# Kernel optimization log

Hardware: AMD Instinct MI355X
Metric: run time of the kernel (lower is better)

Reference implementation:

```python
import jax, jax.numpy as jnp
import numpy as np

NUM_VARS = 64
LAG = 16
H1 = 64
H2 = 1024
NUM_OUT = 1
BATCH = 16384


def setup_inputs() -> dict:
    key = jax.random.key(0)
    ks = jax.random.split(key, 8)

    def xavier(k, shape, fan_in, fan_out):
        std = float(np.sqrt(2.0 / (fan_in + fan_out)))
        return jax.random.normal(k, shape, dtype=jnp.float32) * std

    inputs = jax.random.normal(ks[0], (BATCH, NUM_VARS * LAG), dtype=jnp.float32)
    # Per-variable sub-network weights, batched over the variable axis.
    W1 = xavier(ks[1], (NUM_VARS, LAG, H1), LAG, H1)
    b1 = jnp.full((NUM_VARS, H1), 0.1, dtype=jnp.float32)
    W2 = xavier(ks[2], (NUM_VARS, H1, H1), H1, H1)
    b2 = jnp.full((NUM_VARS, H1), 0.1, dtype=jnp.float32)
    imp = (jnp.ones((NUM_VARS,), dtype=jnp.float32) / NUM_VARS
           + 1e-5 * jax.random.normal(ks[3], (NUM_VARS,), dtype=jnp.float32))
    W3 = xavier(ks[4], (NUM_VARS * H1, H2), NUM_VARS * H1, H2)
    b3 = jnp.full((H2,), 0.1, dtype=jnp.float32)
    W4 = xavier(ks[5], (H2, NUM_OUT), H2, NUM_OUT)
    b4 = jnp.full((NUM_OUT,), 0.1, dtype=jnp.float32)
    return {"inputs": inputs, "W1": W1, "b1": b1, "W2": W2, "b2": b2,
            "imp": imp, "W3": W3, "b3": b3, "W4": W4, "b4": b4}


def reference(inputs, W1, b1, W2, b2, imp, W3, b3, W4, b4):
    B = inputs.shape[0]
    # [B, V*lag] -> [B, V, lag]; slicing inputs[:, lag*i:lag*(i+1)] == x[:, i, :]
    x = inputs.reshape(B, NUM_VARS, LAG)
    # dp = 0.0 -> dropout is identity
    h = jax.nn.relu(jnp.einsum('bvl,vlh->bvh', x, W1) + b1[None])      # [B, V, H1]
    h = jax.nn.relu(jnp.einsum('bvh,vhk->bvk', h, W2) + b2[None])      # [B, V, H1]
    agg = (h * imp[None, :, None]).reshape(B, NUM_VARS * H1)            # weighted concat
    pred = jax.nn.relu(agg @ W3 + b3) @ W4 + b4                        # [B, NUM_OUT]
    return pred
```

## Files before the change

### kernel.cpp

```cpp
#include <hip/hip_runtime.h>
#include <hip/hip_bf16.h>
#include <stdint.h>

#define B_ROWS 16384
#define NVARS 64
#define LAG 16
#define H1 64
#define H2 1024
#define KDIM (NVARS * H1)

typedef __attribute__((ext_vector_type(8))) short short8;
typedef __attribute__((ext_vector_type(4))) short short4v;
typedef __attribute__((ext_vector_type(4))) float f32x4;

typedef __attribute__((address_space(3))) uint8_t lds_u8;
typedef const __attribute__((address_space(1))) uint8_t glob_u8;

__device__ __forceinline__ void gload_lds16(const void* g, void* l) {
    __builtin_amdgcn_global_load_lds((glob_u8*)g, (lds_u8*)l, 16, 0, 0);
}

__device__ __forceinline__ short f2bf_s(float x) {
    __hip_bfloat16 h = __float2bfloat16(x);
    return *(short*)&h;
}
__device__ __forceinline__ float bf_s2f(short s) {
    __hip_bfloat16 h = *(__hip_bfloat16*)&s;
    return __bfloat162float(h);
}

__global__ __launch_bounds__(256) void misc_pre_kernel(
    const float* __restrict__ w3, const float* __restrict__ b4,
    const float* __restrict__ W1, const float* __restrict__ W2,
    __hip_bfloat16* __restrict__ w3t, float* __restrict__ out,
    short* __restrict__ w1bh, short* __restrict__ w1bl,
    short* __restrict__ w2bh, short* __restrict__ w2bl) {
    __shared__ float tile[64][65];
    const int bid = blockIdx.x;
    const int t = threadIdx.x;

    if (bid < 1024) {
        const int k0 = (bid >> 4) * 64;
        const int n0 = (bid & 15) * 64;
        const int c = t & 63, r0 = t >> 6;
#pragma unroll
        for (int i = 0; i < 16; i++) {
            int r = r0 + i * 4;
            tile[r][c] = w3[(size_t)(k0 + r) * H2 + n0 + c];
        }
        __syncthreads();
#pragma unroll
        for (int i = 0; i < 16; i++) {
            int nr = r0 + i * 4;
            w3t[(size_t)(n0 + nr) * KDIM + k0 + c] = __float2bfloat16(tile[c][nr]);
        }
        return;
    }
    if (bid < 1088) {
        out[(bid - 1024) * 256 + t] = b4[0];
        return;
    }

    const int v = bid - 1088;
    for (int idx = t; idx < 64 * 32; idx += 256) {
        int col = idx >> 5, k = idx & 31;
        float wv = W1[((size_t)v * LAG + (k & 15)) * H1 + col];
        short hi = f2bf_s(wv);
        w1bh[((size_t)v * 64 + col) * 40 + k] = hi;
        w1bl[((size_t)v * 64 + col) * 40 + k] = (k < 16) ? f2bf_s(wv - bf_s2f(hi)) : (short)0;
    }
    for (int idx = t; idx < 64 * 64; idx += 256) {
        int col = idx >> 6, k = idx & 63;
        float wv = W2[((size_t)v * H1 + k) * H1 + col];
        short hi = f2bf_s(wv);
        w2bh[((size_t)v * 64 + col) * 72 + k] = hi;
        w2bl[((size_t)v * 64 + col) * 72 + k] = f2bf_s(wv - bf_s2f(hi));
    }
}

__global__ __launch_bounds__(256) void subnets_mfma_kernel(
    const float* __restrict__ inputs, const float* __restrict__ b1g,
    const float* __restrict__ b2g, const float* __restrict__ impg,
    const short* __restrict__ w1bh_g, const short* __restrict__ w1bl_g,
    const short* __restrict__ w2bh_g, const short* __restrict__ w2bl_g,
    __hip_bfloat16* __restrict__ agg) {
    const int v = blockIdx.x >> 7;
    const int b0 = (blockIdx.x & 127) * 128;
    const int t = threadIdx.x;
    const int lane = t & 63, wv = t >> 6;
    const int l15 = lane & 15, g = lane >> 4;

    __shared__ __align__(16) char smem[38912];
    short* xsS   = (short*)smem;
    short* w1bhS = (short*)(smem + 10240);
    short* w1blS = (short*)(smem + 15360);
    short* Hs    = (short*)smem;
    short* w2bhS = (short*)(smem + 20480);
    short* w2blS = (short*)(smem + 29696);

    for (int c = t; c < 320; c += 256) {
        gload_lds16(w1bh_g + (size_t)v * 2560 + c * 8, (char*)w1bhS + c * 16);
        gload_lds16(w1bl_g + (size_t)v * 2560 + c * 8, (char*)w1blS + c * 16);
    }
    for (int c = t; c < 576; c += 256) {
        gload_lds16(w2bh_g + (size_t)v * 4608 + c * 8, (char*)w2bhS + c * 16);
        gload_lds16(w2bl_g + (size_t)v * 4608 + c * 8, (char*)w2blS + c * 16);
    }
#pragma unroll
    for (int i = 0; i < 2; i++) {
        int idx = t + i * 256;
        int row = idx >> 2, seg = idx & 3;
        float4 x4 = *(const float4*)(inputs + (size_t)(b0 + row) * (NVARS * LAG) + v * LAG + seg * 4);
        const float* xp = (const float*)&x4;
        short4v hv, lv;
#pragma unroll
        for (int j = 0; j < 4; j++) {
            short hi = f2bf_s(xp[j]);
            hv[j] = hi;
            lv[j] = f2bf_s(xp[j] - bf_s2f(hi));
        }
        *(short4v*)&xsS[row * 40 + seg * 4] = hv;
        *(short4v*)&xsS[row * 40 + 16 + seg * 4] = lv;
    }
    __syncthreads();

    short8 a1[2], b1hF[4], b1lF[4];
#pragma unroll
    for (int mt = 0; mt < 2; mt++)
        a1[mt] = *(const short8*)&xsS[(wv * 32 + mt * 16 + l15) * 40 + g * 8];
#pragma unroll
    for (int nt = 0; nt < 4; nt++) {
        b1hF[nt] = *(const short8*)&w1bhS[(nt * 16 + l15) * 40 + g * 8];
        b1lF[nt] = *(const short8*)&w1blS[(nt * 16 + l15) * 40 + g * 8];
    }
    f32x4 acc1[2][4];
#pragma unroll
    for (int mt = 0; mt < 2; mt++)
#pragma unroll
        for (int nt = 0; nt < 4; nt++) {
            acc1[mt][nt] = (f32x4){0.f, 0.f, 0.f, 0.f};
            acc1[mt][nt] = __builtin_amdgcn_mfma_f32_16x16x32_bf16(a1[mt], b1hF[nt], acc1[mt][nt], 0, 0, 0);
            acc1[mt][nt] = __builtin_amdgcn_mfma_f32_16x16x32_bf16(a1[mt], b1lF[nt], acc1[mt][nt], 0, 0, 0);
        }
    __syncthreads();

#pragma unroll
    for (int mt = 0; mt < 2; mt++)
#pragma unroll
        for (int nt = 0; nt < 4; nt++) {
            int col = nt * 16 + l15;
            float bias = b1g[v * H1 + col];
#pragma unroll
            for (int r = 0; r < 4; r++) {
                float h = fmaxf(acc1[mt][nt][r] + bias, 0.f);
                int row = wv * 32 + mt * 16 + g * 4 + r;
                Hs[row * 72 + col] = f2bf_s(h);
            }
        }
    __syncthreads();

    short8 a2[2][2], b2hF[4][2], b2lF[4][2];
#pragma unroll
    for (int mt = 0; mt < 2; mt++)
#pragma unroll
        for (int kc = 0; kc < 2; kc++)
            a2[mt][kc] = *(const short8*)&Hs[(wv * 32 + mt * 16 + l15) * 72 + kc * 32 + g * 8];
#pragma unroll
    for (int nt = 0; nt < 4; nt++)
#pragma unroll
        for (int kc = 0; kc < 2; kc++) {
            b2hF[nt][kc] = *(const short8*)&w2bhS[(nt * 16 + l15) * 72 + kc * 32 + g * 8];
            b2lF[nt][kc] = *(const short8*)&w2blS[(nt * 16 + l15) * 72 + kc * 32 + g * 8];
        }
    f32x4 acc2[2][4];
#pragma unroll
    for (int mt = 0; mt < 2; mt++)
#pragma unroll
        for (int nt = 0; nt < 4; nt++) {
            f32x4 a = (f32x4){0.f, 0.f, 0.f, 0.f};
            a = __builtin_amdgcn_mfma_f32_16x16x32_bf16(a2[mt][0], b2hF[nt][0], a, 0, 0, 0);
            a = __builtin_amdgcn_mfma_f32_16x16x32_bf16(a2[mt][1], b2hF[nt][1], a, 0, 0, 0);
            a = __builtin_amdgcn_mfma_f32_16x16x32_bf16(a2[mt][0], b2lF[nt][0], a, 0, 0, 0);
            a = __builtin_amdgcn_mfma_f32_16x16x32_bf16(a2[mt][1], b2lF[nt][1], a, 0, 0, 0);
            acc2[mt][nt] = a;
        }

    const float impv = impg[v];
#pragma unroll
    for (int mt = 0; mt < 2; mt++)
#pragma unroll
        for (int nt = 0; nt < 4; nt++) {
            int col = nt * 16 + l15;
            float bias = b2g[v * H1 + col];
#pragma unroll
            for (int r = 0; r < 4; r++) {
                float o = fmaxf(acc2[mt][nt][r] + bias, 0.f) * impv;
                int row = b0 + wv * 32 + mt * 16 + g * 4 + r;
                agg[(size_t)row * KDIM + v * H1 + col] = __float2bfloat16(o);
            }
        }
}

#define NT 128

__global__ __launch_bounds__(512, 2) void gemm3_kernel(
    const __hip_bfloat16* __restrict__ agg,
    const __hip_bfloat16* __restrict__ w3t,
    const float* __restrict__ b3, const float* __restrict__ W4,
    float* __restrict__ out) {
    const int bid = ((blockIdx.x & 7) << 5) + (blockIdx.x >> 3);
    const int brow = (bid >> 2) * 256;
    const int bcol = (bid & 3) * 256;
    const int t = threadIdx.x;
    const int lane = t & 63;
    const int wid = t >> 6;
    const int wm = wid >> 2, wn = wid & 3;
    const int l15 = lane & 15, g = lane >> 4;

    __shared__ __align__(16) char smem[131072];

    const int c0 = t, c1 = t + 512;
    const int r0 = c0 >> 2, r1 = c1 >> 2;
    const int col0 = ((c0 & 3) * 8) ^ ((r0 & 8) ? 16 : 0);
    const int col1 = ((c1 & 3) * 8) ^ ((r1 & 8) ? 16 : 0);
    const __hip_bfloat16* aS0 = agg + (size_t)(brow + r0) * KDIM + col0;
    const __hip_bfloat16* aS1 = agg + (size_t)(brow + r1) * KDIM + col1;
    const __hip_bfloat16* bS0 = w3t + (size_t)(bcol + r0) * KDIM + col0;
    const __hip_bfloat16* bS1 = w3t + (size_t)(bcol + r1) * KDIM + col1;

#define STAGE_AB(p, kt) do { \
        gload_lds16(aS0 + (kt) * 32, smem + (p) * 32768 + c0 * 16); \
        gload_lds16(aS1 + (kt) * 32, smem + (p) * 32768 + c1 * 16); \
        gload_lds16(bS0 + (kt) * 32, smem + (p) * 32768 + 16384 + c0 * 16); \
        gload_lds16(bS1 + (kt) * 32, smem + (p) * 32768 + 16384 + c1 * 16); } while (0)

    const int coff = (g * 16) ^ ((l15 & 8) ? 32 : 0);
    const int aBase = (wm * 128 + l15) * 64 + coff;
    const int bBase = 16384 + (wn * 64 + l15) * 64 + coff;

#define RD(p, off) (*(const short8*)(smem + (p) * 32768 + (off)))
#define LDFRAGS(FA, FB, p) do { \
        FA[0] = RD(p, aBase + 0 * 1024); FA[1] = RD(p, aBase + 1 * 1024); \
        FA[2] = RD(p, aBase + 2 * 1024); FA[3] = RD(p, aBase + 3 * 1024); \
        FA[4] = RD(p, aBase + 4 * 1024); FA[5] = RD(p, aBase + 5 * 1024); \
        FA[6] = RD(p, aBase + 6 * 1024); FA[7] = RD(p, aBase + 7 * 1024); \
        FB[0] = RD(p, bBase + 0 * 1024); FB[1] = RD(p, bBase + 1 * 1024); \
        FB[2] = RD(p, bBase + 2 * 1024); FB[3] = RD(p, bBase + 3 * 1024); } while (0)

#define MM(FA, FB) do { \
        __builtin_amdgcn_s_setprio(1); \
        _Pragma("unroll") \
        for (int mm = 0; mm < 8; mm++) \
            _Pragma("unroll") \
            for (int nn = 0; nn < 4; nn++) \
                acc[mm][nn] = __builtin_amdgcn_mfma_f32_16x16x32_bf16( \
                    FA[mm], FB[nn], acc[mm][nn], 0, 0, 0); \
        __builtin_amdgcn_s_setprio(0); } while (0)

#define TILE(FAc, FBc, FAn, FBn, tn, DOPREF, DOSTAGE, kt3, VMSTR) do { \
        if (DOPREF) LDFRAGS(FAn, FBn, (tn) & 3); \
        if (DOSTAGE) STAGE_AB((kt3) & 3, kt3); \
        MM(FAc, FBc); \
        asm volatile(VMSTR ::: "memory"); \
        __builtin_amdgcn_s_barrier(); \
        __builtin_amdgcn_sched_barrier(0); } while (0)

    short8 fa0[8], fb0[4], fa1[8], fb1[4];
    f32x4 acc[8][4];
#pragma unroll
    for (int m = 0; m < 8; m++)
#pragma unroll
        for (int n = 0; n < 4; n++) acc[m][n] = (f32x4){0.f, 0.f, 0.f, 0.f};

    STAGE_AB(0, 0);
    STAGE_AB(1, 1);
    STAGE_AB(2, 2);
    asm volatile("s_waitcnt vmcnt(4)" ::: "memory");
    __builtin_amdgcn_s_barrier();
    __builtin_amdgcn_sched_barrier(0);
    LDFRAGS(fa0, fb0, 0);

#pragma unroll 4
    for (int tt = 0; tt < NT - 4; ++tt) {
        if (tt & 1) TILE(fa1, fb1, fa0, fb0, tt + 1, 1, 1, tt + 3, "s_waitcnt vmcnt(4)");
        else        TILE(fa0, fb0, fa1, fb1, tt + 1, 1, 1, tt + 3, "s_waitcnt vmcnt(4)");
    }
    TILE(fa0, fb0, fa1, fb1, 125, 1, 1, 127, "s_waitcnt vmcnt(4)");
    TILE(fa1, fb1, fa0, fb0, 126, 1, 0, 0,   "s_waitcnt vmcnt(0)");
    TILE(fa0, fb0, fa1, fb1, 127, 1, 0, 0,   "s_waitcnt vmcnt(0)");
    MM(fa1, fb1);

    float bias[4], w4v[4];
#pragma unroll
    for (int n = 0; n < 4; n++) {
        int col = bcol + wn * 64 + n * 16 + l15;
        bias[n] = b3[col];
        w4v[n] = W4[col];
    }
#pragma unroll
    for (int m = 0; m < 8; m++) {
        float pr0 = 0.f, pr1 = 0.f, pr2 = 0.f, pr3 = 0.f;
#pragma unroll
        for (int n = 0; n < 4; n++) {
            pr0 += fmaxf(acc[m][n][0] + bias[n], 0.f) * w4v[n];
            pr1 += fmaxf(acc[m][n][1] + bias[n], 0.f) * w4v[n];
            pr2 += fmaxf(acc[m][n][2] + bias[n], 0.f) * w4v[n];
            pr3 += fmaxf(acc[m][n][3] + bias[n], 0.f) * w4v[n];
        }
#pragma unroll
        for (int mask = 1; mask < 16; mask <<= 1) {
            pr0 += __shfl_xor(pr0, mask, 64);
            pr1 += __shfl_xor(pr1, mask, 64);
            pr2 += __shfl_xor(pr2, mask, 64);
            pr3 += __shfl_xor(pr3, mask, 64);
        }
        if (l15 == 0) {
            int row = brow + wm * 128 + m * 16 + g * 4;
            atomicAdd(&out[row + 0], pr0);
            atomicAdd(&out[row + 1], pr1);
            atomicAdd(&out[row + 2], pr2);
            atomicAdd(&out[row + 3], pr3);
        }
    }
}

extern "C" void kernel_launch(void* const* d_in, const int* in_sizes, int n_in,
                              void* d_out, int out_size, void* d_ws, size_t ws_size,
                              hipStream_t stream) {
    const float* inputs = (const float*)d_in[0];
    const float* W1 = (const float*)d_in[1];
    const float* b1 = (const float*)d_in[2];
    const float* W2 = (const float*)d_in[3];
    const float* b2 = (const float*)d_in[4];
    const float* imp = (const float*)d_in[5];
    const float* W3 = (const float*)d_in[6];
    const float* b3 = (const float*)d_in[7];
    const float* W4 = (const float*)d_in[8];
    const float* b4 = (const float*)d_in[9];
    float* out = (float*)d_out;

    char* ws = (char*)d_ws;
    const size_t agg_bytes = (size_t)B_ROWS * KDIM * 2;
    const size_t w3t_bytes = (size_t)H2 * KDIM * 2;
    const size_t w1b_bytes = (size_t)NVARS * 64 * 40 * 2;
    const size_t w2b_bytes = (size_t)NVARS * 64 * 72 * 2;

    __hip_bfloat16* agg = (__hip_bfloat16*)ws;
    __hip_bfloat16* w3t = (__hip_bfloat16*)(ws + agg_bytes);
    short* w1bh = (short*)(ws + agg_bytes + w3t_bytes);
    short* w1bl = (short*)(ws + agg_bytes + w3t_bytes + w1b_bytes);
    short* w2bh = (short*)(ws + agg_bytes + w3t_bytes + 2 * w1b_bytes);
    short* w2bl = (short*)(ws + agg_bytes + w3t_bytes + 2 * w1b_bytes + w2b_bytes);

    hipLaunchKernelGGL(misc_pre_kernel, dim3(1152), dim3(256), 0, stream,
                       W3, b4, W1, W2, w3t, out, w1bh, w1bl, w2bh, w2bl);
    hipLaunchKernelGGL(subnets_mfma_kernel, dim3(NVARS * (B_ROWS / 128)), dim3(256), 0, stream,
                       inputs, b1, b2, imp, w1bh, w1bl, w2bh, w2bl, agg);
    hipLaunchKernelGGL(gemm3_kernel, dim3((B_ROWS / 256) * (H2 / 256)), dim3(512), 0, stream,
                       agg, w3t, b3, W4, out);
}
```

Measured before the change: 183.8 us.

## Load GEMM3 B fragments directly from global into registers, halve LDS staging

The W3 operand is no longer staged through LDS. Each wave now loads its B fragments straight from global memory into registers, two k-tiles ahead, while only the A tile keeps the 4-stage LDS ring, which halves shared memory to 64KB. A-fragment register double-buffering is dropped: A fragments are read from LDS right before each MFMA batch. The aim is to cut LDS traffic and footprint. The cost is uncoalesced-ish global loads for B, duplicated across the wm waves, and LDS read latency exposed with no prefetch.

Result: slower. 223.8 us (+21.8%).

```diff
diff --git a/kernel.cpp b/kernel.cpp
--- a/kernel.cpp
+++ b/kernel.cpp
@@ -217,7 +217,7 @@
     const int wm = wid >> 2, wn = wid & 3;
     const int l15 = lane & 15, g = lane >> 4;
 
-    __shared__ __align__(16) char smem[131072];
+    __shared__ __align__(16) char smem[65536];
 
     const int c0 = t, c1 = t + 512;
     const int r0 = c0 >> 2, r1 = c1 >> 2;
@@ -225,70 +225,69 @@
     const int col1 = ((c1 & 3) * 8) ^ ((r1 & 8) ? 16 : 0);
     const __hip_bfloat16* aS0 = agg + (size_t)(brow + r0) * KDIM + col0;
     const __hip_bfloat16* aS1 = agg + (size_t)(brow + r1) * KDIM + col1;
-    const __hip_bfloat16* bS0 = w3t + (size_t)(bcol + r0) * KDIM + col0;
-    const __hip_bfloat16* bS1 = w3t + (size_t)(bcol + r1) * KDIM + col1;
-
-#define STAGE_AB(p, kt) do { \
-        gload_lds16(aS0 + (kt) * 32, smem + (p) * 32768 + c0 * 16); \
-        gload_lds16(aS1 + (kt) * 32, smem + (p) * 32768 + c1 * 16); \
-        gload_lds16(bS0 + (kt) * 32, smem + (p) * 32768 + 16384 + c0 * 16); \
-        gload_lds16(bS1 + (kt) * 32, smem + (p) * 32768 + 16384 + c1 * 16); } while (0)
+
+#define STAGE_A(p, kt) do { \
+        gload_lds16(aS0 + (kt) * 32, smem + (p) * 16384 + c0 * 16); \
+        gload_lds16(aS1 + (kt) * 32, smem + (p) * 16384 + c1 * 16); } while (0)
 
     const int coff = (g * 16) ^ ((l15 & 8) ? 32 : 0);
     const int aBase = (wm * 128 + l15) * 64 + coff;
-    const int bBase = 16384 + (wn * 64 + l15) * 64 + coff;
-
-#define RD(p, off) (*(const short8*)(smem + (p) * 32768 + (off)))
-#define LDFRAGS(FA, FB, p) do { \
-        FA[0] = RD(p, aBase + 0 * 1024); FA[1] = RD(p, aBase + 1 * 1024); \
-        FA[2] = RD(p, aBase + 2 * 1024); FA[3] = RD(p, aBase + 3 * 1024); \
-        FA[4] = RD(p, aBase + 4 * 1024); FA[5] = RD(p, aBase + 5 * 1024); \
-        FA[6] = RD(p, aBase + 6 * 1024); FA[7] = RD(p, aBase + 7 * 1024); \
-        FB[0] = RD(p, bBase + 0 * 1024); FB[1] = RD(p, bBase + 1 * 1024); \
-        FB[2] = RD(p, bBase + 2 * 1024); FB[3] = RD(p, bBase + 3 * 1024); } while (0)
-
-#define MM(FA, FB) do { \
+#define LDA(i, p) fa[i] = *(const short8*)(smem + (p) * 16384 + aBase + (i) * 1024)
+
+    const __hip_bfloat16* bP = w3t + (size_t)(bcol + wn * 64 + l15) * KDIM + g * 8;
+#define LDFB(FB, kt) do { \
+        FB[0] = *(const short8*)(bP + (size_t)(kt) * 32); \
+        FB[1] = *(const short8*)(bP + (size_t)(kt) * 32 + 16 * KDIM); \
+        FB[2] = *(const short8*)(bP + (size_t)(kt) * 32 + 32 * KDIM); \
+        FB[3] = *(const short8*)(bP + (size_t)(kt) * 32 + 48 * KDIM); } while (0)
+
+#define MM(FB) do { \
         __builtin_amdgcn_s_setprio(1); \
         _Pragma("unroll") \
         for (int mm = 0; mm < 8; mm++) \
             _Pragma("unroll") \
             for (int nn = 0; nn < 4; nn++) \
                 acc[mm][nn] = __builtin_amdgcn_mfma_f32_16x16x32_bf16( \
-                    FA[mm], FB[nn], acc[mm][nn], 0, 0, 0); \
+                    fa[mm], FB[nn], acc[mm][nn], 0, 0, 0); \
         __builtin_amdgcn_s_setprio(0); } while (0)
 
-#define TILE(FAc, FBc, FAn, FBn, tn, DOPREF, DOSTAGE, kt3, VMSTR) do { \
-        if (DOPREF) LDFRAGS(FAn, FBn, (tn) & 3); \
-        if (DOSTAGE) STAGE_AB((kt3) & 3, kt3); \
-        MM(FAc, FBc); \
+#define TILE(FB, p, DOSTAGE, kt3, DOFB, ktfb, VMSTR) do { \
+        if (DOSTAGE) STAGE_A((kt3) & 3, kt3); \
+        LDA(0, p); LDA(1, p); LDA(2, p); LDA(3, p); \
+        LDA(4, p); LDA(5, p); LDA(6, p); LDA(7, p); \
+        MM(FB); \
+        if (DOFB) LDFB(FB, ktfb); \
         asm volatile(VMSTR ::: "memory"); \
         __builtin_amdgcn_s_barrier(); \
         __builtin_amdgcn_sched_barrier(0); } while (0)
 
-    short8 fa0[8], fb0[4], fa1[8], fb1[4];
+    short8 fa[8], fb0[4], fb1[4];
     f32x4 acc[8][4];
 #pragma unroll
     for (int m = 0; m < 8; m++)
 #pragma unroll
         for (int n = 0; n < 4; n++) acc[m][n] = (f32x4){0.f, 0.f, 0.f, 0.f};
 
-    STAGE_AB(0, 0);
-    STAGE_AB(1, 1);
-    STAGE_AB(2, 2);
+    STAGE_A(0, 0);
+    STAGE_A(1, 1);
+    STAGE_A(2, 2);
+    LDFB(fb0, 0);
+    LDFB(fb1, 1);
     asm volatile("s_waitcnt vmcnt(4)" ::: "memory");
     __builtin_amdgcn_s_barrier();
     __builtin_amdgcn_sched_barrier(0);
-    LDFRAGS(fa0, fb0, 0);
-
-#pragma unroll 4
-    for (int tt = 0; tt < NT - 4; ++tt) {
-        if (tt & 1) TILE(fa1, fb1, fa0, fb0, tt + 1, 1, 1, tt + 3, "s_waitcnt vmcnt(4)");
-        else        TILE(fa0, fb0, fa1, fb1, tt + 1, 1, 1, tt + 3, "s_waitcnt vmcnt(4)");
-    }
-    TILE(fa0, fb0, fa1, fb1, 125, 1, 1, 127, "s_waitcnt vmcnt(4)");
-    TILE(fa1, fb1, fa0, fb0, 126, 1, 0, 0,   "s_waitcnt vmcnt(0)");
-    TILE(fa0, fb0, fa1, fb1, 127, 1, 0, 0,   "s_waitcnt vmcnt(0)");
-    MM(fa1, fb1);
+
+    for (int t2 = 0; t2 < 62; ++t2) {
+        const int tt = t2 * 2;
+        TILE(fb0, tt & 3,       1, tt + 3, 1, tt + 2, "s_waitcnt vmcnt(6)");
+        TILE(fb1, (tt + 1) & 3, 1, tt + 4, 1, tt + 3, "s_waitcnt vmcnt(6)");
+    }
+    TILE(fb0, 0, 1, 127, 1, 126, "s_waitcnt vmcnt(6)");
+    TILE(fb1, 1, 0, 0,   1, 127, "s_waitcnt vmcnt(4)");
+    TILE(fb0, 2, 0, 0,   0, 0,   "s_waitcnt vmcnt(0)");
+    LDA(0, 3); LDA(1, 3); LDA(2, 3); LDA(3, 3);
+    LDA(4, 3); LDA(5, 3); LDA(6, 3); LDA(7, 3);
+    MM(fb1);
 
     float bias[4], w4v[4];
 #pragma unroll
```

## Use 4-wave blocks with 128x128 per-wave tiles in the final GEMM

Applied to the files above, without the earlier changes.

Halves the gemm3 block from 512 to 256 threads (4 waves, 2x2) and gives each wave a 128x128 output tile with 8x8 MFMA accumulators instead of 128x64. This raises arithmetic intensity per LDS fragment read and halves the number of waves contending for LDS bandwidth. Each thread now issues 8 global-to-LDS loads per stage, and the wait counts are adjusted to match. The cost is much higher register pressure (256 accumulator floats per thread) and only one wave per SIMD, so less latency hiding.

New measurement: 183.3 us. Within noise of the previous version (-0.3%).

```diff
diff --git a/kernel.cpp b/kernel.cpp
--- a/kernel.cpp
+++ b/kernel.cpp
@@ -203,7 +203,7 @@
 
 #define NT 128
 
-__global__ __launch_bounds__(512, 2) void gemm3_kernel(
+__global__ __launch_bounds__(256, 1) void gemm3_kernel(
     const __hip_bfloat16* __restrict__ agg,
     const __hip_bfloat16* __restrict__ w3t,
     const float* __restrict__ b3, const float* __restrict__ W4,
@@ -214,86 +214,95 @@
     const int t = threadIdx.x;
     const int lane = t & 63;
     const int wid = t >> 6;
-    const int wm = wid >> 2, wn = wid & 3;
+    const int wm = wid >> 1, wn = wid & 1;
     const int l15 = lane & 15, g = lane >> 4;
 
     __shared__ __align__(16) char smem[131072];
 
-    const int c0 = t, c1 = t + 512;
-    const int r0 = c0 >> 2, r1 = c1 >> 2;
-    const int col0 = ((c0 & 3) * 8) ^ ((r0 & 8) ? 16 : 0);
-    const int col1 = ((c1 & 3) * 8) ^ ((r1 & 8) ? 16 : 0);
-    const __hip_bfloat16* aS0 = agg + (size_t)(brow + r0) * KDIM + col0;
-    const __hip_bfloat16* aS1 = agg + (size_t)(brow + r1) * KDIM + col1;
-    const __hip_bfloat16* bS0 = w3t + (size_t)(bcol + r0) * KDIM + col0;
-    const __hip_bfloat16* bS1 = w3t + (size_t)(bcol + r1) * KDIM + col1;
+    const int r0 = t >> 2;
+    const int col0 = ((t & 3) * 8) ^ ((r0 & 8) ? 16 : 0);
+    const __hip_bfloat16* aSrc = agg + (size_t)(brow + r0) * KDIM + col0;
+    const __hip_bfloat16* bSrc = w3t + (size_t)(bcol + r0) * KDIM + col0;
 
 #define STAGE_AB(p, kt) do { \
-        gload_lds16(aS0 + (kt) * 32, smem + (p) * 32768 + c0 * 16); \
-        gload_lds16(aS1 + (kt) * 32, smem + (p) * 32768 + c1 * 16); \
-        gload_lds16(bS0 + (kt) * 32, smem + (p) * 32768 + 16384 + c0 * 16); \
-        gload_lds16(bS1 + (kt) * 32, smem + (p) * 32768 + 16384 + c1 * 16); } while (0)
+        gload_lds16(aSrc + (size_t)(kt) * 32,                  smem + (p) * 32768 + t * 16); \
+        gload_lds16(aSrc + (size_t)(kt) * 32 +  64 * KDIM,     smem + (p) * 32768 + t * 16 + 4096); \
+        gload_lds16(aSrc + (size_t)(kt) * 32 + 128 * KDIM,     smem + (p) * 32768 + t * 16 + 8192); \
+        gload_lds16(aSrc + (size_t)(kt) * 32 + 192 * KDIM,     smem + (p) * 32768 + t * 16 + 12288); \
+        gload_lds16(bSrc + (size_t)(kt) * 32,                  smem + (p) * 32768 + 16384 + t * 16); \
+        gload_lds16(bSrc + (size_t)(kt) * 32 +  64 * KDIM,     smem + (p) * 32768 + 16384 + t * 16 + 4096); \
+        gload_lds16(bSrc + (size_t)(kt) * 32 + 128 * KDIM,     smem + (p) * 32768 + 16384 + t * 16 + 8192); \
+        gload_lds16(bSrc + (size_t)(kt) * 32 + 192 * KDIM,     smem + (p) * 32768 + 16384 + t * 16 + 12288); } while (0)
 
     const int coff = (g * 16) ^ ((l15 & 8) ? 32 : 0);
     const int aBase = (wm * 128 + l15) * 64 + coff;
-    const int bBase = 16384 + (wn * 64 + l15) * 64 + coff;
-
-#define RD(p, off) (*(const short8*)(smem + (p) * 32768 + (off)))
+    const int bBase = 16384 + (wn * 128 + l15) * 64 + coff;
+
 #define LDFRAGS(FA, FB, p) do { \
-        FA[0] = RD(p, aBase + 0 * 1024); FA[1] = RD(p, aBase + 1 * 1024); \
-        FA[2] = RD(p, aBase + 2 * 1024); FA[3] = RD(p, aBase + 3 * 1024); \
-        FA[4] = RD(p, aBase + 4 * 1024); FA[5] = RD(p, aBase + 5 * 1024); \
-        FA[6] = RD(p, aBase + 6 * 1024); FA[7] = RD(p, aBase + 7 * 1024); \
-        FB[0] = RD(p, bBase + 0 * 1024); FB[1] = RD(p, bBase + 1 * 1024); \
-        FB[2] = RD(p, bBase + 2 * 1024); FB[3] = RD(p, bBase + 3 * 1024); } while (0)
+        FA[0] = *(const short8*)(smem + (p) * 32768 + aBase + 0 * 1024); \
+        FA[1] = *(const short8*)(smem + (p) * 32768 + aBase + 1 * 1024); \
+        FA[2] = *(const short8*)(smem + (p) * 32768 + aBase + 2 * 1024); \
+        FA[3] = *(const short8*)(smem + (p) * 32768 + aBase + 3 * 1024); \
+        FA[4] = *(const short8*)(smem + (p) * 32768 + aBase + 4 * 1024); \
+        FA[5] = *(const short8*)(smem + (p) * 32768 + aBase + 5 * 1024); \
+        FA[6] = *(const short8*)(smem + (p) * 32768 + aBase + 6 * 1024); \
+        FA[7] = *(const short8*)(smem + (p) * 32768 + aBase + 7 * 1024); \
+        FB[0] = *(const short8*)(smem + (p) * 32768 + bBase + 0 * 1024); \
+        FB[1] = *(const short8*)(smem + (p) * 32768 + bBase + 1 * 1024); \
+        FB[2] = *(const short8*)(smem + (p) * 32768 + bBase + 2 * 1024); \
+        FB[3] = *(const short8*)(smem + (p) * 32768 + bBase + 3 * 1024); \
+        FB[4] = *(const short8*)(smem + (p) * 32768 + bBase + 4 * 1024); \
+        FB[5] = *(const short8*)(smem + (p) * 32768 + bBase + 5 * 1024); \
+        FB[6] = *(const short8*)(smem + (p) * 32768 + bBase + 6 * 1024); \
+        FB[7] = *(const short8*)(smem + (p) * 32768 + bBase + 7 * 1024); } while (0)
 
 #define MM(FA, FB) do { \
         __builtin_amdgcn_s_setprio(1); \
         _Pragma("unroll") \
         for (int mm = 0; mm < 8; mm++) \
             _Pragma("unroll") \
-            for (int nn = 0; nn < 4; nn++) \
+            for (int nn = 0; nn < 8; nn++) \
                 acc[mm][nn] = __builtin_amdgcn_mfma_f32_16x16x32_bf16( \
                     FA[mm], FB[nn], acc[mm][nn], 0, 0, 0); \
         __builtin_amdgcn_s_setprio(0); } while (0)
 
-#define TILE(FAc, FBc, FAn, FBn, tn, DOPREF, DOSTAGE, kt3, VMSTR) do { \
-        if (DOPREF) LDFRAGS(FAn, FBn, (tn) & 3); \
+#define TILE(FAc, FBc, FAn, FBn, pn, DOPREF, DOSTAGE, kt3, VMSTR) do { \
+        if (DOPREF) LDFRAGS(FAn, FBn, pn); \
         if (DOSTAGE) STAGE_AB((kt3) & 3, kt3); \
         MM(FAc, FBc); \
         asm volatile(VMSTR ::: "memory"); \
         __builtin_amdgcn_s_barrier(); \
         __builtin_amdgcn_sched_barrier(0); } while (0)
 
-    short8 fa0[8], fb0[4], fa1[8], fb1[4];
-    f32x4 acc[8][4];
+    short8 faA[8], fbA[8], faB[8], fbB[8];
+    f32x4 acc[8][8];
 #pragma unroll
     for (int m = 0; m < 8; m++)
 #pragma unroll
-        for (int n = 0; n < 4; n++) acc[m][n] = (f32x4){0.f, 0.f, 0.f, 0.f};
+        for (int n = 0; n < 8; n++) acc[m][n] = (f32x4){0.f, 0.f, 0.f, 0.f};
 
     STAGE_AB(0, 0);
     STAGE_AB(1, 1);
     STAGE_AB(2, 2);
-    asm volatile("s_waitcnt vmcnt(4)" ::: "memory");
+    asm volatile("s_waitcnt vmcnt(8)" ::: "memory");
     __builtin_amdgcn_s_barrier();
     __builtin_amdgcn_sched_barrier(0);
-    LDFRAGS(fa0, fb0, 0);
-
-#pragma unroll 4
-    for (int tt = 0; tt < NT - 4; ++tt) {
-        if (tt & 1) TILE(fa1, fb1, fa0, fb0, tt + 1, 1, 1, tt + 3, "s_waitcnt vmcnt(4)");
-        else        TILE(fa0, fb0, fa1, fb1, tt + 1, 1, 1, tt + 3, "s_waitcnt vmcnt(4)");
-    }
-    TILE(fa0, fb0, fa1, fb1, 125, 1, 1, 127, "s_waitcnt vmcnt(4)");
-    TILE(fa1, fb1, fa0, fb0, 126, 1, 0, 0,   "s_waitcnt vmcnt(0)");
-    TILE(fa0, fb0, fa1, fb1, 127, 1, 0, 0,   "s_waitcnt vmcnt(0)");
-    MM(fa1, fb1);
-
-    float bias[4], w4v[4];
-#pragma unroll
-    for (int n = 0; n < 4; n++) {
-        int col = bcol + wn * 64 + n * 16 + l15;
+    LDFRAGS(faA, fbA, 0);
+
+    for (int t2 = 0; t2 < 62; ++t2) {
+        const int tt = t2 * 2;
+        TILE(faA, fbA, faB, fbB, (tt + 1) & 3, 1, 1, tt + 3, "s_waitcnt vmcnt(8)");
+        TILE(faB, fbB, faA, fbA, (tt + 2) & 3, 1, 1, tt + 4, "s_waitcnt vmcnt(8)");
+    }
+    TILE(faA, fbA, faB, fbB, 1, 1, 1, 127, "s_waitcnt vmcnt(8)");
+    TILE(faB, fbB, faA, fbA, 2, 1, 0, 0,   "s_waitcnt vmcnt(0)");
+    TILE(faA, fbA, faB, fbB, 3, 1, 0, 0,   "s_waitcnt vmcnt(0)");
+    MM(faB, fbB);
+
+    float bias[8], w4v[8];
+#pragma unroll
+    for (int n = 0; n < 8; n++) {
+        int col = bcol + wn * 128 + n * 16 + l15;
         bias[n] = b3[col];
         w4v[n] = W4[col];
     }
@@ -301,7 +310,7 @@
     for (int m = 0; m < 8; m++) {
         float pr0 = 0.f, pr1 = 0.f, pr2 = 0.f, pr3 = 0.f;
 #pragma unroll
-        for (int n = 0; n < 4; n++) {
+        for (int n = 0; n < 8; n++) {
             pr0 += fmaxf(acc[m][n][0] + bias[n], 0.f) * w4v[n];
             pr1 += fmaxf(acc[m][n][1] + bias[n], 0.f) * w4v[n];
             pr2 += fmaxf(acc[m][n][2] + bias[n], 0.f) * w4v[n];
@@ -356,6 +365,6 @@
                        W3, b4, W1, W2, w3t, out, w1bh, w1bl, w2bh, w2bl);
     hipLaunchKernelGGL(subnets_mfma_kernel, dim3(NVARS * (B_ROWS / 128)), dim3(256), 0, stream,
                        inputs, b1, b2, imp, w1bh, w1bl, w2bh, w2bl, agg);
-    hipLaunchKernelGGL(gemm3_kernel, dim3((B_ROWS / 256) * (H2 / 256)), dim3(512), 0, stream,
+    hipLaunchKernelGGL(gemm3_kernel, dim3((B_ROWS / 256) * (H2 / 256)), dim3(256), 0, stream,
                        agg, w3t, b3, W4, out);
 }
```

## Merge W3 transpose into subnet kernel and re-pipeline GEMM3 with half-tile phases

Applied to the files above, without the earlier changes.

The W3 transpose and output init move out of the prep kernel and into the subnet launch as extra leading blocks, so that work overlaps the per-variable MLP blocks and the small prep kernel only packs W1/W2. The GEMM3 main loop is restructured from a 4-stage full-tile ring with double-buffered register fragments into an 8-slot A/B LDS layout. Each k-tile is processed in two half-M phases, with staggered per-operand global-to-LDS loads and barriers around each phase. This lowers register pressure and interleaves loads more finely, but it adds many more barriers per k-step.

After: 163.6 us. -11.0%, faster.

```diff
diff --git a/kernel.cpp b/kernel.cpp
--- a/kernel.cpp
+++ b/kernel.cpp
@@ -29,39 +29,11 @@
     return __bfloat162float(h);
 }
 
-__global__ __launch_bounds__(256) void misc_pre_kernel(
-    const float* __restrict__ w3, const float* __restrict__ b4,
+__global__ __launch_bounds__(256) void prep_w12_kernel(
     const float* __restrict__ W1, const float* __restrict__ W2,
-    __hip_bfloat16* __restrict__ w3t, float* __restrict__ out,
     short* __restrict__ w1bh, short* __restrict__ w1bl,
     short* __restrict__ w2bh, short* __restrict__ w2bl) {
-    __shared__ float tile[64][65];
-    const int bid = blockIdx.x;
-    const int t = threadIdx.x;
-
-    if (bid < 1024) {
-        const int k0 = (bid >> 4) * 64;
-        const int n0 = (bid & 15) * 64;
-        const int c = t & 63, r0 = t >> 6;
-#pragma unroll
-        for (int i = 0; i < 16; i++) {
-            int r = r0 + i * 4;
-            tile[r][c] = w3[(size_t)(k0 + r) * H2 + n0 + c];
-        }
-        __syncthreads();
-#pragma unroll
-        for (int i = 0; i < 16; i++) {
-            int nr = r0 + i * 4;
-            w3t[(size_t)(n0 + nr) * KDIM + k0 + c] = __float2bfloat16(tile[c][nr]);
-        }
-        return;
-    }
-    if (bid < 1088) {
-        out[(bid - 1024) * 256 + t] = b4[0];
-        return;
-    }
-
-    const int v = bid - 1088;
+    const int v = blockIdx.x, t = threadIdx.x;
     for (int idx = t; idx < 64 * 32; idx += 256) {
         int col = idx >> 5, k = idx & 31;
         float wv = W1[((size_t)v * LAG + (k & 15)) * H1 + col];
@@ -78,19 +50,47 @@
     }
 }
 
-__global__ __launch_bounds__(256) void subnets_mfma_kernel(
+__global__ __launch_bounds__(256) void subnets_fused_kernel(
     const float* __restrict__ inputs, const float* __restrict__ b1g,
     const float* __restrict__ b2g, const float* __restrict__ impg,
     const short* __restrict__ w1bh_g, const short* __restrict__ w1bl_g,
     const short* __restrict__ w2bh_g, const short* __restrict__ w2bl_g,
+    const float* __restrict__ w3, const float* __restrict__ b4,
+    __hip_bfloat16* __restrict__ w3t, float* __restrict__ out,
     __hip_bfloat16* __restrict__ agg) {
-    const int v = blockIdx.x >> 7;
-    const int b0 = (blockIdx.x & 127) * 128;
+    __shared__ __align__(16) char smem[38912];
+    const int bid = blockIdx.x;
     const int t = threadIdx.x;
+
+    if (bid < 1024) {
+        float (*tile)[65] = (float (*)[65])smem;
+        const int k0 = (bid >> 4) * 64;
+        const int n0 = (bid & 15) * 64;
+        const int c = t & 63, r0 = t >> 6;
+#pragma unroll
+        for (int i = 0; i < 16; i++) {
+            int r = r0 + i * 4;
+            tile[r][c] = w3[(size_t)(k0 + r) * H2 + n0 + c];
+        }
+        __syncthreads();
+#pragma unroll
+        for (int i = 0; i < 16; i++) {
+            int nr = r0 + i * 4;
+            w3t[(size_t)(n0 + nr) * KDIM + k0 + c] = __float2bfloat16(tile[c][nr]);
+        }
+        return;
+    }
+    if (bid < 1088) {
+        out[(bid - 1024) * 256 + t] = b4[0];
+        return;
+    }
+
+    const int sbid = bid - 1088;
+    const int v = sbid >> 7;
+    const int b0 = (sbid & 127) * 128;
     const int lane = t & 63, wv = t >> 6;
     const int l15 = lane & 15, g = lane >> 4;
 
-    __shared__ __align__(16) char smem[38912];
     short* xsS   = (short*)smem;
     short* w1bhS = (short*)(smem + 10240);
     short* w1blS = (short*)(smem + 15360);
@@ -201,7 +201,14 @@
         }
 }
 
-#define NT 128
+#define D0A0 0
+#define D0A1 16384
+#define D0B0 32768
+#define D0B1 49152
+#define D1A0 65536
+#define D1A1 81920
+#define D1B0 98304
+#define D1B1 114688
 
 __global__ __launch_bounds__(512, 2) void gemm3_kernel(
     const __hip_bfloat16* __restrict__ agg,
@@ -228,67 +235,88 @@
     const __hip_bfloat16* bS0 = w3t + (size_t)(bcol + r0) * KDIM + col0;
     const __hip_bfloat16* bS1 = w3t + (size_t)(bcol + r1) * KDIM + col1;
 
-#define STAGE_AB(p, kt) do { \
-        gload_lds16(aS0 + (kt) * 32, smem + (p) * 32768 + c0 * 16); \
-        gload_lds16(aS1 + (kt) * 32, smem + (p) * 32768 + c1 * 16); \
-        gload_lds16(bS0 + (kt) * 32, smem + (p) * 32768 + 16384 + c0 * 16); \
-        gload_lds16(bS1 + (kt) * 32, smem + (p) * 32768 + 16384 + c1 * 16); } while (0)
+#define SA(rb, kt) do { \
+        gload_lds16(aS0 + (size_t)(kt) * 32, smem + (rb) + c0 * 16); \
+        gload_lds16(aS1 + (size_t)(kt) * 32, smem + (rb) + c1 * 16); } while (0)
+#define SB(rb, kt) do { \
+        gload_lds16(bS0 + (size_t)(kt) * 32, smem + (rb) + c0 * 16); \
+        gload_lds16(bS1 + (size_t)(kt) * 32, smem + (rb) + c1 * 16); } while (0)
 
     const int coff = (g * 16) ^ ((l15 & 8) ? 32 : 0);
     const int aBase = (wm * 128 + l15) * 64 + coff;
-    const int bBase = 16384 + (wn * 64 + l15) * 64 + coff;
-
-#define RD(p, off) (*(const short8*)(smem + (p) * 32768 + (off)))
-#define LDFRAGS(FA, FB, p) do { \
-        FA[0] = RD(p, aBase + 0 * 1024); FA[1] = RD(p, aBase + 1 * 1024); \
-        FA[2] = RD(p, aBase + 2 * 1024); FA[3] = RD(p, aBase + 3 * 1024); \
-        FA[4] = RD(p, aBase + 4 * 1024); FA[5] = RD(p, aBase + 5 * 1024); \
-        FA[6] = RD(p, aBase + 6 * 1024); FA[7] = RD(p, aBase + 7 * 1024); \
-        FB[0] = RD(p, bBase + 0 * 1024); FB[1] = RD(p, bBase + 1 * 1024); \
-        FB[2] = RD(p, bBase + 2 * 1024); FB[3] = RD(p, bBase + 3 * 1024); } while (0)
-
-#define MM(FA, FB) do { \
-        __builtin_amdgcn_s_setprio(1); \
+    const int bBase = (wn * 64 + l15) * 64 + coff;
+
+#define LDA4(rb, MH) do { \
+        fa[0] = *(const short8*)(smem + (rb) + aBase + ((MH) * 4 + 0) * 1024); \
+        fa[1] = *(const short8*)(smem + (rb) + aBase + ((MH) * 4 + 1) * 1024); \
+        fa[2] = *(const short8*)(smem + (rb) + aBase + ((MH) * 4 + 2) * 1024); \
+        fa[3] = *(const short8*)(smem + (rb) + aBase + ((MH) * 4 + 3) * 1024); } while (0)
+#define LDB4(FB, rb) do { \
+        FB[0] = *(const short8*)(smem + (rb) + bBase + 0 * 1024); \
+        FB[1] = *(const short8*)(smem + (rb) + bBase + 1 * 1024); \
+        FB[2] = *(const short8*)(smem + (rb) + bBase + 2 * 1024); \
+        FB[3] = *(const short8*)(smem + (rb) + bBase + 3 * 1024); } while (0)
+
+#define MFMA16(MH, FB) \
         _Pragma("unroll") \
-        for (int mm = 0; mm < 8; mm++) \
+        for (int mm = 0; mm < 4; mm++) { \
             _Pragma("unroll") \
             for (int nn = 0; nn < 4; nn++) \
-                acc[mm][nn] = __builtin_amdgcn_mfma_f32_16x16x32_bf16( \
-                    FA[mm], FB[nn], acc[mm][nn], 0, 0, 0); \
-        __builtin_amdgcn_s_setprio(0); } while (0)
-
-#define TILE(FAc, FBc, FAn, FBn, tn, DOPREF, DOSTAGE, kt3, VMSTR) do { \
-        if (DOPREF) LDFRAGS(FAn, FBn, (tn) & 3); \
-        if (DOSTAGE) STAGE_AB((kt3) & 3, kt3); \
-        MM(FAc, FBc); \
-        asm volatile(VMSTR ::: "memory"); \
+                acc[(MH) * 4 + mm][nn] = __builtin_amdgcn_mfma_f32_16x16x32_bf16( \
+                    fa[mm], FB[nn], acc[(MH) * 4 + mm][nn], 0, 0, 0); \
+        }
+
+#define PHX(MH, FB) do { \
         __builtin_amdgcn_s_barrier(); \
-        __builtin_amdgcn_sched_barrier(0); } while (0)
-
-    short8 fa0[8], fb0[4], fa1[8], fb1[4];
+        asm volatile("s_waitcnt lgkmcnt(0)" ::: "memory"); \
+        __builtin_amdgcn_sched_barrier(0); \
+        __builtin_amdgcn_s_setprio(1); \
+        MFMA16(MH, FB) \
+        __builtin_amdgcn_s_setprio(0); \
+        __builtin_amdgcn_s_barrier(); } while (0)
+
+#define PHXV(MH, FB, VM) do { \
+        __builtin_amdgcn_s_barrier(); \
+        asm volatile("s_waitcnt lgkmcnt(0)" ::: "memory"); \
+        __builtin_amdgcn_sched_barrier(0); \
+        __builtin_amdgcn_s_setprio(1); \
+        MFMA16(MH, FB) \
+        __builtin_amdgcn_s_setprio(0); \
+        asm volatile(VM ::: "memory"); \
+        __builtin_amdgcn_s_barrier(); } while (0)
+
+    short8 fa[4], fbk0[4], fbk1[4];
     f32x4 acc[8][4];
 #pragma unroll
     for (int m = 0; m < 8; m++)
 #pragma unroll
         for (int n = 0; n < 4; n++) acc[m][n] = (f32x4){0.f, 0.f, 0.f, 0.f};
 
-    STAGE_AB(0, 0);
-    STAGE_AB(1, 1);
-    STAGE_AB(2, 2);
-    asm volatile("s_waitcnt vmcnt(4)" ::: "memory");
+    SA(D0A0, 0); SA(D0A1, 1); SB(D0B0, 0); SB(D0B1, 1);
+    SA(D1A0, 2); SB(D1B0, 2); SB(D1B1, 3);
+    asm volatile("s_waitcnt vmcnt(6)" ::: "memory");
     __builtin_amdgcn_s_barrier();
     __builtin_amdgcn_sched_barrier(0);
-    LDFRAGS(fa0, fb0, 0);
-
-#pragma unroll 4
-    for (int tt = 0; tt < NT - 4; ++tt) {
-        if (tt & 1) TILE(fa1, fb1, fa0, fb0, tt + 1, 1, 1, tt + 3, "s_waitcnt vmcnt(4)");
-        else        TILE(fa0, fb0, fa1, fb1, tt + 1, 1, 1, tt + 3, "s_waitcnt vmcnt(4)");
-    }
-    TILE(fa0, fb0, fa1, fb1, 125, 1, 1, 127, "s_waitcnt vmcnt(4)");
-    TILE(fa1, fb1, fa0, fb0, 126, 1, 0, 0,   "s_waitcnt vmcnt(0)");
-    TILE(fa0, fb0, fa1, fb1, 127, 1, 0, 0,   "s_waitcnt vmcnt(0)");
-    MM(fa1, fb1);
+
+    for (int i = 0; i < 31; ++i) {
+        const int k4 = i * 4;
+        LDB4(fbk0, D0B0); LDA4(D0A0, 0); SA(D1A1, k4 + 3);  PHX(0, fbk0);
+        LDA4(D0A0, 1);    SB(D0B0, k4 + 4);                 PHX(1, fbk0);
+        LDB4(fbk1, D0B1); LDA4(D0A1, 0); SA(D0A0, k4 + 4);  PHX(0, fbk1);
+        LDA4(D0A1, 1);    SB(D0B1, k4 + 5);                 PHXV(1, fbk1, "s_waitcnt vmcnt(6)");
+        LDB4(fbk0, D1B0); LDA4(D1A0, 0); SA(D0A1, k4 + 5);  PHX(0, fbk0);
+        LDA4(D1A0, 1);    SB(D1B0, k4 + 6);                 PHX(1, fbk0);
+        LDB4(fbk1, D1B1); LDA4(D1A1, 0); SA(D1A0, k4 + 6);  PHX(0, fbk1);
+        LDA4(D1A1, 1);    SB(D1B1, k4 + 7);                 PHXV(1, fbk1, "s_waitcnt vmcnt(6)");
+    }
+    LDB4(fbk0, D0B0); LDA4(D0A0, 0); SA(D1A1, 127);         PHX(0, fbk0);
+    LDA4(D0A0, 1);                                          PHX(1, fbk0);
+    LDB4(fbk1, D0B1); LDA4(D0A1, 0);                        PHX(0, fbk1);
+    LDA4(D0A1, 1);                                          PHXV(1, fbk1, "s_waitcnt vmcnt(0)");
+    LDB4(fbk0, D1B0); LDA4(D1A0, 0);                        PHX(0, fbk0);
+    LDA4(D1A0, 1);                                          PHX(1, fbk0);
+    LDB4(fbk1, D1B1); LDA4(D1A1, 0);                        PHX(0, fbk1);
+    LDA4(D1A1, 1);                                          PHX(1, fbk1);
 
     float bias[4], w4v[4];
 #pragma unroll
@@ -352,10 +380,11 @@
     short* w2bh = (short*)(ws + agg_bytes + w3t_bytes + 2 * w1b_bytes);
     short* w2bl = (short*)(ws + agg_bytes + w3t_bytes + 2 * w1b_bytes + w2b_bytes);
 
-    hipLaunchKernelGGL(misc_pre_kernel, dim3(1152), dim3(256), 0, stream,
-                       W3, b4, W1, W2, w3t, out, w1bh, w1bl, w2bh, w2bl);
-    hipLaunchKernelGGL(subnets_mfma_kernel, dim3(NVARS * (B_ROWS / 128)), dim3(256), 0, stream,
-                       inputs, b1, b2, imp, w1bh, w1bl, w2bh, w2bl, agg);
+    hipLaunchKernelGGL(prep_w12_kernel, dim3(NVARS), dim3(256), 0, stream,
+                       W1, W2, w1bh, w1bl, w2bh, w2bl);
+    hipLaunchKernelGGL(subnets_fused_kernel, dim3(1088 + NVARS * (B_ROWS / 128)), dim3(256), 0, stream,
+                       inputs, b1, b2, imp, w1bh, w1bl, w2bh, w2bl,
+                       W3, b4, w3t, out, agg);
     hipLaunchKernelGGL(gemm3_kernel, dim3((B_ROWS / 256) * (H2 / 256)), dim3(512), 0, stream,
                        agg, w3t, b3, W4, out);
 }
```
